# Performance work log

Hardware: AMD Instinct MI355X
Metric: run time of the kernel (lower is better)

## Reference

```python
import jax, jax.numpy as jnp
from jax import lax
import numpy as np

B, N, K = 8, 4096, 64          # clouds, points per cloud, max neighbors
N1, N2 = N // 2, N // 8        # fps ratio 0.5, then 0.25
R1, R2 = 0.2, 0.4              # ball-query radii


def setup_inputs() -> dict:
    key = jax.random.key(0)
    ks = jax.random.split(key, 7)
    def w(k, i, o):
        return jax.random.normal(k, (i, o), jnp.float32) / np.sqrt(i).astype(np.float32)
    return {
        "pos": jax.random.uniform(ks[0], (B, N, 3), jnp.float32),
        "w1a": w(ks[1], 3, 64),    "b1a": jnp.zeros(64, jnp.float32),
        "w1b": w(ks[2], 64, 64),   "b1b": jnp.zeros(64, jnp.float32),
        "w2a": w(ks[3], 67, 128),  "b2a": jnp.zeros(128, jnp.float32),
        "w2b": w(ks[4], 128, 128), "b2b": jnp.zeros(128, jnp.float32),
        "w3a": w(ks[5], 131, 256), "b3a": jnp.zeros(256, jnp.float32),
        "w3b": w(ks[6], 256, 1024),"b3b": jnp.zeros(1024, jnp.float32),
    }


def fps(pos, n_samples):
    # farthest point sampling, deterministic start at index 0. pos: [n, 3]
    d0 = jnp.sum((pos - pos[0]) ** 2, axis=-1)
    def step(mind, _):
        nxt = jnp.argmax(mind)
        d = jnp.sum((pos - pos[nxt]) ** 2, axis=-1)
        return jnp.minimum(mind, d), nxt
    _, idxs = lax.scan(step, d0, None, length=n_samples - 1)
    return jnp.concatenate([jnp.zeros((1,), idxs.dtype), idxs])


def ball_query(centers, pts, r):
    # up to K neighbors within radius r (nearest-first); centers are a subset of pts
    d2 = jnp.sum((centers[:, None, :] - pts[None, :, :]) ** 2, axis=-1)  # [M, n]
    neg = jnp.where(d2 <= r * r, -d2, -jnp.inf)
    vals, nbr = lax.top_k(neg, K)
    return nbr, vals > -jnp.inf  # [M, K] indices, validity mask


def mlp(x, w1, b1, w2, b2, relu_last):
    h = jax.nn.relu(x @ w1 + b1) @ w2 + b2
    return jax.nn.relu(h) if relu_last else h


def masked_max(h, mask):
    # max over neighbor axis; every center has itself as a valid neighbor
    return jnp.max(jnp.where(mask[..., None], h, -jnp.inf), axis=1)


def reference(pos, w1a, b1a, w1b, b1b, w2a, b2a, w2b, b2b, w3a, b3a, w3b, b3b):
    def single(p):  # p: [N, 3]
        # SA1: x is None -> per-edge input is relative position only
        idx1 = fps(p, N1)
        c1 = p[idx1]                                   # [N1, 3]
        nbr1, m1 = ball_query(c1, p, R1)               # [N1, K]
        rel1 = p[nbr1] - c1[:, None, :]                # [N1, K, 3]
        x1 = masked_max(mlp(rel1, w1a, b1a, w1b, b1b, True), m1)   # [N1, 64]
        # SA2: per-edge input is [x_j, pos_j - pos_i]
        idx2 = fps(c1, N2)
        c2 = c1[idx2]                                  # [N2, 3]
        nbr2, m2 = ball_query(c2, c1, R2)              # [N2, K]
        feat2 = jnp.concatenate([x1[nbr2], c1[nbr2] - c2[:, None, :]], axis=-1)  # [N2,K,67]
        x2 = masked_max(mlp(feat2, w2a, b2a, w2b, b2b, True), m2)  # [N2, 128]
        # Global SA: MLP on [x, pos] then global max pool
        g = mlp(jnp.concatenate([x2, c2], axis=-1), w3a, b3a, w3b, b3b, False)   # [N2,1024]
        return jnp.max(g, axis=0)                      # [1024]
    return jax.vmap(single)(pos)                       # [B, 1024]
```

## Files before the change

### kernel.cpp

```cpp
#include <hip/hip_runtime.h>
#include <cstdint>
#include <cstddef>


static constexpr int Bc = 8;
static constexpr int Np = 4096;
static constexpr int Kn = 64;
static constexpr int M1 = 2048;
static constexpr int M2 = 512;
static constexpr int LDX = 132;

#define DEVINL __device__ __forceinline__

DEVINL float d2_exact(float ax, float ay, float az, float bx, float by, float bz) {
    float dx = __fsub_rn(ax, bx);
    float dy = __fsub_rn(ay, by);
    float dz = __fsub_rn(az, bz);
    float xx = __fmul_rn(dx, dx);
    float yy = __fmul_rn(dy, dy);
    float zz = __fmul_rn(dz, dz);
    return __fadd_rn(__fadd_rn(xx, yy), zz);
}

template <int CTRL, int RM, int BM>
DEVINL unsigned long long dpp_max_step(unsigned long long k) {
    unsigned lo = (unsigned)k, hi = (unsigned)(k >> 32);
    unsigned slo = (unsigned)__builtin_amdgcn_update_dpp(0, (int)lo, CTRL, RM, BM, true);
    unsigned shi = (unsigned)__builtin_amdgcn_update_dpp(0, (int)hi, CTRL, RM, BM, true);
    unsigned long long s = ((unsigned long long)shi << 32) | (unsigned long long)slo;
    return s > k ? s : k;
}

DEVINL unsigned long long wave_max_u64_dpp(unsigned long long k) {
    k = dpp_max_step<0x111, 0xf, 0xf>(k);
    k = dpp_max_step<0x112, 0xf, 0xf>(k);
    k = dpp_max_step<0x114, 0xf, 0xf>(k);
    k = dpp_max_step<0x118, 0xf, 0xf>(k);
    k = dpp_max_step<0x142, 0xa, 0xf>(k);
    k = dpp_max_step<0x143, 0xc, 0xf>(k);
    return k;
}

DEVINL unsigned mort3(unsigned v) {
    return (v & 1u) | ((v & 2u) << 2) | ((v & 4u) << 4);
}

DEVINL unsigned cell_of(float x, float y, float z) {
    int ix = (int)(x * 8.0f); ix = ix < 0 ? 0 : (ix > 7 ? 7 : ix);
    int iy = (int)(y * 8.0f); iy = iy < 0 ? 0 : (iy > 7 ? 7 : iy);
    int iz = (int)(z * 8.0f); iz = iz < 0 ? 0 : (iz > 7 ? 7 : iz);
    return mort3((unsigned)ix) | (mort3((unsigned)iy) << 1) | (mort3((unsigned)iz) << 2);
}

DEVINL unsigned* scan512(unsigned* h0, unsigned* h1, int t) {
    unsigned* src = h0; unsigned* dst = h1;
    for (int d = 1; d < 512; d <<= 1) {
        unsigned v = src[t];
        if (t >= d) v += src[t - d];
        dst[t] = v;
        __syncthreads();
        unsigned* tmp = src; src = dst; dst = tmp;
    }
    return src;
}

__global__ __launch_bounds__(512)
void fps2x_kernel(const float* __restrict__ pos, float* __restrict__ c1,
                  float* __restrict__ c2, float* __restrict__ X) {
    constexpr int NT = 512;
    __shared__ float scx[Np], scy[Np], scz[Np];
    __shared__ unsigned spk[Np];
    __shared__ float s2c[M1 * 3];
    __shared__ unsigned h0[512], h1[512];
    __shared__ unsigned long long slots[3];
    const int b = blockIdx.x;
    const int t = threadIdx.x;
    const int lane = t & 63;

    {
        constexpr int PT = Np / NT;
        const float* base = pos + (size_t)b * Np * 3;
        float gx[PT], gy[PT], gz[PT];
        unsigned gc[PT];
        #pragma unroll
        for (int j = 0; j < PT; ++j) {
            int p = j * NT + t;
            gx[j] = base[p * 3 + 0];
            gy[j] = base[p * 3 + 1];
            gz[j] = base[p * 3 + 2];
            gc[j] = cell_of(gx[j], gy[j], gz[j]);
        }
        float x0 = base[0], y0 = base[1], z0 = base[2];
        h0[t] = 0;
        if (t == 0) { slots[0] = 0; slots[1] = 0; slots[2] = 0; }
        __syncthreads();
        #pragma unroll
        for (int j = 0; j < PT; ++j) atomicAdd(&h0[gc[j]], 1u);
        __syncthreads();
        unsigned cnt = h0[t];
        unsigned* inc = scan512(h0, h1, t);
        inc[t] -= cnt;
        __syncthreads();
        #pragma unroll
        for (int j = 0; j < PT; ++j) {
            unsigned p = atomicAdd(&inc[gc[j]], 1u);
            scx[p] = gx[j]; scy[p] = gy[j]; scz[p] = gz[j];
            spk[p] = ((0xFFFu - (unsigned)(j * NT + t)) << 12) | p;
        }
        __syncthreads();

        float px[PT], py[PT], pz[PT], mind[PT];
        unsigned oi[PT];
        #pragma unroll
        for (int j = 0; j < PT; ++j) {
            int p = t * PT + j;
            px[j] = scx[p]; py[j] = scy[p]; pz[j] = scz[p];
            oi[j] = spk[p];
        }
        float lox = px[0], hix = px[0], loy = py[0], hiy = py[0], loz = pz[0], hiz = pz[0];
        #pragma unroll
        for (int j = 1; j < PT; ++j) {
            lox = fminf(lox, px[j]); hix = fmaxf(hix, px[j]);
            loy = fminf(loy, py[j]); hiy = fmaxf(hiy, py[j]);
            loz = fminf(loz, pz[j]); hiz = fmaxf(hiz, pz[j]);
        }

        unsigned long long ck = 0;
        #pragma unroll
        for (int j = 0; j < PT; ++j) {
            float d = d2_exact(px[j], py[j], pz[j], x0, y0, z0);
            mind[j] = d;
            unsigned long long kj =
                ((unsigned long long)__float_as_uint(d) << 24) | (unsigned long long)oi[j];
            if (kj > ck) ck = kj;
        }
        float bmax = __uint_as_float((unsigned)(ck >> 24));
        unsigned long long wkey = wave_max_u64_dpp(ck);
        if (lane == 63) atomicMax(&slots[1], wkey);
        if (t == 0) {
            c1[((size_t)b * M1) * 3 + 0] = x0;
            c1[((size_t)b * M1) * 3 + 1] = y0;
            c1[((size_t)b * M1) * 3 + 2] = z0;
            s2c[0] = x0; s2c[1] = y0; s2c[2] = z0;
        }
        int rd = 1, wr = 2, rs = 0;
        for (int s = 1; s < M1; ++s) {
            __syncthreads();
            unsigned long long km = slots[rd];
            if (t == 0) slots[rs] = 0;
            unsigned spos = (unsigned)km & 0xFFFu;
            float cx = scx[spos], cy = scy[spos], cz = scz[spos];
            if (t == 0) {
                c1[((size_t)b * M1 + s) * 3 + 0] = cx;
                c1[((size_t)b * M1 + s) * 3 + 1] = cy;
                c1[((size_t)b * M1 + s) * 3 + 2] = cz;
                s2c[s * 3 + 0] = cx; s2c[s * 3 + 1] = cy; s2c[s * 3 + 2] = cz;
            }
            float dxv = fmaxf(fmaxf(lox - cx, cx - hix), 0.0f);
            float dyv = fmaxf(fmaxf(loy - cy, cy - hiy), 0.0f);
            float dzv = fmaxf(fmaxf(loz - cz, cz - hiz), 0.0f);
            float L = dxv * dxv + dyv * dyv + dzv * dzv;
            bool fire = (L * 0.999f <= bmax);
            if (fire) {
                unsigned long long nck = 0;
                #pragma unroll
                for (int j = 0; j < PT; ++j) {
                    float d = d2_exact(px[j], py[j], pz[j], cx, cy, cz);
                    float m = fminf(mind[j], d);
                    mind[j] = m;
                    unsigned long long kj =
                        ((unsigned long long)__float_as_uint(m) << 24) | (unsigned long long)oi[j];
                    if (kj > nck) nck = kj;
                }
                ck = nck;
                bmax = __uint_as_float((unsigned)(ck >> 24));
            }
            if (__ballot(fire) != 0ull) wkey = wave_max_u64_dpp(ck);
            if (lane == 63) atomicMax(&slots[wr], wkey);
            int nrd = wr; wr = rs; rs = rd; rd = nrd;
        }
    }
    __syncthreads();

    {
        constexpr int PT = M1 / NT;
        float gx[PT], gy[PT], gz[PT];
        unsigned gc[PT];
        #pragma unroll
        for (int j = 0; j < PT; ++j) {
            int p = j * NT + t;
            gx[j] = s2c[p * 3 + 0];
            gy[j] = s2c[p * 3 + 1];
            gz[j] = s2c[p * 3 + 2];
            gc[j] = cell_of(gx[j], gy[j], gz[j]);
        }
        float x0 = s2c[0], y0 = s2c[1], z0 = s2c[2];
        h0[t] = 0;
        if (t == 0) { slots[0] = 0; slots[1] = 0; slots[2] = 0; }
        __syncthreads();
        #pragma unroll
        for (int j = 0; j < PT; ++j) atomicAdd(&h0[gc[j]], 1u);
        __syncthreads();
        unsigned cnt = h0[t];
        unsigned* inc = scan512(h0, h1, t);
        inc[t] -= cnt;
        __syncthreads();
        #pragma unroll
        for (int j = 0; j < PT; ++j) {
            unsigned p = atomicAdd(&inc[gc[j]], 1u);
            scx[p] = gx[j]; scy[p] = gy[j]; scz[p] = gz[j];
            spk[p] = ((0xFFFu - (unsigned)(j * NT + t)) << 12) | p;
        }
        __syncthreads();

        float px[PT], py[PT], pz[PT], mind[PT];
        unsigned oi[PT];
        #pragma unroll
        for (int j = 0; j < PT; ++j) {
            int p = t * PT + j;
            px[j] = scx[p]; py[j] = scy[p]; pz[j] = scz[p];
            oi[j] = spk[p];
        }
        float lox = px[0], hix = px[0], loy = py[0], hiy = py[0], loz = pz[0], hiz = pz[0];
        #pragma unroll
        for (int j = 1; j < PT; ++j) {
            lox = fminf(lox, px[j]); hix = fmaxf(hix, px[j]);
            loy = fminf(loy, py[j]); hiy = fmaxf(hiy, py[j]);
            loz = fminf(loz, pz[j]); hiz = fmaxf(hiz, pz[j]);
        }

        unsigned long long ck = 0;
        #pragma unroll
        for (int j = 0; j < PT; ++j) {
            float d = d2_exact(px[j], py[j], pz[j], x0, y0, z0);
            mind[j] = d;
            unsigned long long kj =
                ((unsigned long long)__float_as_uint(d) << 24) | (unsigned long long)oi[j];
            if (kj > ck) ck = kj;
        }
        float bmax = __uint_as_float((unsigned)(ck >> 24));
        unsigned long long wkey = wave_max_u64_dpp(ck);
        if (lane == 63) atomicMax(&slots[1], wkey);
        if (t == 0) {
            c2[((size_t)b * M2) * 3 + 0] = x0;
            c2[((size_t)b * M2) * 3 + 1] = y0;
            c2[((size_t)b * M2) * 3 + 2] = z0;
            float* xr = X + (size_t)(b * M2) * LDX;
            xr[128] = x0; xr[129] = y0; xr[130] = z0;
        }
        int rd = 1, wr = 2, rs = 0;
        for (int s = 1; s < M2; ++s) {
            __syncthreads();
            unsigned long long km = slots[rd];
            if (t == 0) slots[rs] = 0;
            unsigned spos = (unsigned)km & 0xFFFu;
            float cx = scx[spos], cy = scy[spos], cz = scz[spos];
            if (t == 0) {
                c2[((size_t)b * M2 + s) * 3 + 0] = cx;
                c2[((size_t)b * M2 + s) * 3 + 1] = cy;
                c2[((size_t)b * M2 + s) * 3 + 2] = cz;
                float* xr = X + (size_t)(b * M2 + s) * LDX;
                xr[128] = cx; xr[129] = cy; xr[130] = cz;
            }
            float dxv = fmaxf(fmaxf(lox - cx, cx - hix), 0.0f);
            float dyv = fmaxf(fmaxf(loy - cy, cy - hiy), 0.0f);
            float dzv = fmaxf(fmaxf(loz - cz, cz - hiz), 0.0f);
            float L = dxv * dxv + dyv * dyv + dzv * dzv;
            bool fire = (L * 0.999f <= bmax);
            if (fire) {
                unsigned long long nck = 0;
                #pragma unroll
                for (int j = 0; j < PT; ++j) {
                    float d = d2_exact(px[j], py[j], pz[j], cx, cy, cz);
                    float m = fminf(mind[j], d);
                    mind[j] = m;
                    unsigned long long kj =
                        ((unsigned long long)__float_as_uint(m) << 24) | (unsigned long long)oi[j];
                    if (kj > nck) nck = kj;
                }
                ck = nck;
                bmax = __uint_as_float((unsigned)(ck >> 24));
            }
            if (__ballot(fire) != 0ull) wkey = wave_max_u64_dpp(ck);
            if (lane == 63) atomicMax(&slots[wr], wkey);
            int nrd = wr; wr = rs; rs = rd; rd = nrd;
        }
    }
}

template <int NPT>
__global__ __launch_bounds__(256)
void bq_kernel(const float* __restrict__ pts, const float* __restrict__ ctr,
               int mshift, float r2, int* __restrict__ nbr) {
    constexpr int CH = NPT / 64;
    constexpr int CAP = 1024;
    __shared__ uint2 cbuf[4][CAP];
    const int lane = threadIdx.x & 63;
    const int wl = threadIdx.x >> 6;
    int w = __builtin_amdgcn_readfirstlane((int)(blockIdx.x * 4 + wl));
    const int b = w >> mshift;
    const float* pb = pts + (size_t)b * NPT * 3;
    const float* cp = ctr + (size_t)w * 3;
    float cx = cp[0], cy = cp[1], cz = cp[2];
    const unsigned r2b = __float_as_uint(r2);

    unsigned ub[CH];
    int cnt = 0;
    #pragma unroll
    for (int j = 0; j < CH; ++j) {
        int p = j * 64 + lane;
        float d = d2_exact(pb[p * 3 + 0], pb[p * 3 + 1], pb[p * 3 + 2], cx, cy, cz);
        ub[j] = __float_as_uint(d);
        cnt += __popcll(__ballot(ub[j] <= r2b));
    }
    int* out = nbr + (size_t)w * Kn;
    const unsigned long long lml = (1ull << lane) - 1ull;

    if (cnt <= Kn) {
        int basep = 0;
        #pragma unroll
        for (int j = 0; j < CH; ++j) {
            bool v = ub[j] <= r2b;
            unsigned long long mk = __ballot(v);
            if (v) out[basep + __popcll(mk & lml)] = j * 64 + lane;
            basep += __popcll(mk);
        }
        if (lane >= cnt) out[lane] = -1;
    } else if (cnt <= CAP) {
        uint2* buf = cbuf[wl];
        int basep = 0;
        #pragma unroll
        for (int j = 0; j < CH; ++j) {
            bool v = ub[j] <= r2b;
            unsigned long long mk = __ballot(v);
            if (v) buf[basep + __popcll(mk & lml)] =
                       make_uint2(ub[j], (unsigned)(j * 64 + lane));
            basep += __popcll(mk);
        }
        const int C2 = (cnt + 63) >> 6;
        unsigned cb[CAP / 64], ci[CAP / 64];
        #pragma unroll
        for (int e = 0; e < CAP / 64; ++e) {
            if (e >= C2) break;
            int p = e * 64 + lane;
            uint2 v = buf[p];
            cb[e] = (p < cnt) ? v.x : 0xFFFFFFFFu;
            ci[e] = v.y;
        }
        unsigned lo = 0, hi = r2b;
        while (lo < hi) {
            unsigned mid = lo + ((hi - lo) >> 1);
            int c = 0;
            #pragma unroll
            for (int e = 0; e < CAP / 64; ++e) {
                if (e >= C2) break;
                c += __popcll(__ballot(cb[e] <= mid));
            }
            if (c >= Kn) hi = mid; else lo = mid + 1;
        }
        const unsigned tt = lo;
        int cntLess = 0;
        #pragma unroll
        for (int e = 0; e < CAP / 64; ++e) {
            if (e >= C2) break;
            cntLess += __popcll(__ballot(cb[e] < tt));
        }
        const int quota = Kn - cntLess;
        int baseLt = 0, eqseen = 0;
        #pragma unroll
        for (int e = 0; e < CAP / 64; ++e) {
            if (e >= C2) break;
            bool lt = cb[e] < tt;
            bool eq = cb[e] == tt;
            unsigned long long mlt = __ballot(lt);
            unsigned long long meq = __ballot(eq);
            if (lt) out[baseLt + __popcll(mlt & lml)] = (int)ci[e];
            if (eq) {
                int rr = eqseen + __popcll(meq & lml);
                if (rr < quota) out[cntLess + rr] = (int)ci[e];
            }
            baseLt += __popcll(mlt);
            eqseen += __popcll(meq);
        }
    } else {
        unsigned lo = 0, hi = r2b;
        while (lo < hi) {
            unsigned mid = lo + ((hi - lo) >> 1);
            int c = 0;
            #pragma unroll
            for (int j = 0; j < CH; ++j) c += __popcll(__ballot(ub[j] <= mid));
            if (c >= Kn) hi = mid; else lo = mid + 1;
        }
        const unsigned tt = lo;
        int cntLess = 0;
        #pragma unroll
        for (int j = 0; j < CH; ++j) cntLess += __popcll(__ballot(ub[j] < tt));
        const int quota = Kn - cntLess;
        int baseLt = 0, eqseen = 0;
        #pragma unroll
        for (int j = 0; j < CH; ++j) {
            bool lt = ub[j] < tt;
            bool eq = ub[j] == tt;
            unsigned long long mlt = __ballot(lt);
            unsigned long long meq = __ballot(eq);
            if (lt) out[baseLt + __popcll(mlt & lml)] = j * 64 + lane;
            if (eq) {
                int rr = eqseen + __popcll(meq & lml);
                if (rr < quota) out[cntLess + rr] = j * 64 + lane;
            }
            baseLt += __popcll(mlt);
            eqseen += __popcll(meq);
        }
    }
}

__global__ __launch_bounds__(256)
void mlp1_kernel(const float* __restrict__ pos, const float* __restrict__ c1,
                 const int* __restrict__ nbr, const float* __restrict__ w1aT,
                 const float* __restrict__ w1bT, const float* __restrict__ b1b,
                 float* __restrict__ x1) {
    const int lane = threadIdx.x & 63;
    int w = __builtin_amdgcn_readfirstlane((int)(blockIdx.x * 4 + (threadIdx.x >> 6)));
    const int b = w >> 11;
    const int ii = nbr[(size_t)w * Kn + lane];
    const bool valid = ii >= 0;
    const int i2 = valid ? ii : 0;
    const float* pp = pos + ((size_t)b * Np + i2) * 3;
    const float* cc = c1 + (size_t)w * 3;
    float rx = pp[0] - cc[0], ry = pp[1] - cc[1], rz = pp[2] - cc[2];
    float h1[64];
    #pragma unroll
    for (int h = 0; h < 64; ++h) {
        float4 wv = ((const float4*)w1aT)[h];
        float a = fmaf(rx, wv.x, fmaf(ry, wv.y, fmaf(rz, wv.z, wv.w)));
        h1[h] = fmaxf(a, 0.0f);
    }
    float* orow = x1 + (size_t)w * 64;
    for (int c4 = 0; c4 < 16; ++c4) {
        float v4[4];
        #pragma unroll
        for (int cq = 0; cq < 4; ++cq) {
            int c = c4 * 4 + cq;
            float acc = b1b[c];
            const float4* wr = (const float4*)(w1bT + (size_t)c * 64);
            #pragma unroll
            for (int q = 0; q < 16; ++q) {
                float4 wv = wr[q];
                acc = fmaf(h1[4 * q + 0], wv.x, acc);
                acc = fmaf(h1[4 * q + 1], wv.y, acc);
                acc = fmaf(h1[4 * q + 2], wv.z, acc);
                acc = fmaf(h1[4 * q + 3], wv.w, acc);
            }
            float v = fmaxf(acc, 0.0f);
            v = valid ? v : -__builtin_inff();
            #pragma unroll
            for (int o = 32; o > 0; o >>= 1) v = fmaxf(v, __shfl_xor(v, o, 64));
            v4[cq] = v;
        }
        if (lane == 0)
            ((float4*)orow)[c4] = make_float4(v4[0], v4[1], v4[2], v4[3]);
    }
}

__global__ __launch_bounds__(256)
void mlp2_kernel(const float* __restrict__ x1, const float* __restrict__ c1,
                 const float* __restrict__ c2, const int* __restrict__ nbr2,
                 const float* __restrict__ w2aT, const float* __restrict__ w2bT,
                 const float* __restrict__ b2b, float* __restrict__ X) {
    const int lane = threadIdx.x & 63;
    int w = __builtin_amdgcn_readfirstlane((int)(blockIdx.x * 4 + (threadIdx.x >> 6)));
    const int b = w >> 9;
    const int ii = nbr2[(size_t)w * Kn + lane];
    const bool valid = ii >= 0;
    const int i2 = valid ? ii : 0;

    float x[68];
    const float4* xr = (const float4*)(x1 + ((size_t)b * M1 + i2) * 64);
    #pragma unroll
    for (int q = 0; q < 16; ++q) {
        float4 v = xr[q];
        x[4 * q + 0] = v.x; x[4 * q + 1] = v.y;
        x[4 * q + 2] = v.z; x[4 * q + 3] = v.w;
    }
    const float* cc = c2 + (size_t)w * 3;
    const float* cp = c1 + ((size_t)b * M1 + i2) * 3;
    x[64] = cp[0] - cc[0];
    x[65] = cp[1] - cc[1];
    x[66] = cp[2] - cc[2];
    x[67] = 0.0f;

    float h1[128];
    #pragma unroll
    for (int h = 0; h < 128; ++h) {
        const float4* r4 = (const float4*)(w2aT + (size_t)h * 80);
        float acc = 0.0f;
        #pragma unroll
        for (int q = 0; q < 16; ++q) {
            float4 wv = r4[q];
            acc = fmaf(x[4 * q + 0], wv.x, acc);
            acc = fmaf(x[4 * q + 1], wv.y, acc);
            acc = fmaf(x[4 * q + 2], wv.z, acc);
            acc = fmaf(x[4 * q + 3], wv.w, acc);
        }
        float4 tl = r4[16];
        acc = fmaf(x[64], tl.x, acc);
        acc = fmaf(x[65], tl.y, acc);
        acc = fmaf(x[66], tl.z, acc);
        acc += tl.w;
        h1[h] = fmaxf(acc, 0.0f);
    }
    float* orow = X + (size_t)w * LDX;
    for (int c4 = 0; c4 < 32; ++c4) {
        float v4[4];
        #pragma unroll
        for (int cq = 0; cq < 4; ++cq) {
            int c = c4 * 4 + cq;
            float acc = b2b[c];
            const float4* wr = (const float4*)(w2bT + (size_t)c * 128);
            #pragma unroll
            for (int q = 0; q < 32; ++q) {
                float4 wv = wr[q];
                acc = fmaf(h1[4 * q + 0], wv.x, acc);
                acc = fmaf(h1[4 * q + 1], wv.y, acc);
                acc = fmaf(h1[4 * q + 2], wv.z, acc);
                acc = fmaf(h1[4 * q + 3], wv.w, acc);
            }
            float v = fmaxf(acc, 0.0f);
            v = valid ? v : -__builtin_inff();
            #pragma unroll
            for (int o = 32; o > 0; o >>= 1) v = fmaxf(v, __shfl_xor(v, o, 64));
            v4[cq] = v;
        }
        if (lane == 0) {
            orow[c4 * 4 + 0] = v4[0]; orow[c4 * 4 + 1] = v4[1];
            orow[c4 * 4 + 2] = v4[2]; orow[c4 * 4 + 3] = v4[3];
        }
    }
}

__global__ __launch_bounds__(256)
void gemm1_kernel(const float* __restrict__ X, const float* __restrict__ w3a,
                  const float* __restrict__ b3a, float* __restrict__ H) {
    const int r = blockIdx.x;
    const int c = threadIdx.x;
    const float* xr = X + (size_t)r * LDX;
    float acc = b3a[c];
    for (int i = 0; i < 131; ++i)
        acc = fmaf(xr[i], w3a[(size_t)i * 256 + c], acc);
    H[(size_t)r * 256 + c] = fmaxf(acc, 0.0f);
}

__global__ __launch_bounds__(256)
void gemm2_kernel(const float* __restrict__ H, const float* __restrict__ w3b,
                  float* __restrict__ part) {
    __shared__ float As[32][33];
    __shared__ float Bs[32][64];
    __shared__ float red[8][64];
    const int bidx = blockIdx.x;
    const int nt = bidx & 15;
    const int mt = (bidx >> 4) & 15;
    const int b = bidx >> 8;
    const int row0 = b * M2 + mt * 32;
    const int col0 = nt * 64;
    const int t = threadIdx.x;
    const int rg = t >> 5, cg = t & 31;

    float acc[4][2] = {{0.f, 0.f}, {0.f, 0.f}, {0.f, 0.f}, {0.f, 0.f}};
    for (int k0 = 0; k0 < 256; k0 += 32) {
        #pragma unroll
        for (int q = 0; q < 4; ++q) {
            int id = t + q * 256;
            As[id >> 5][id & 31] = H[(size_t)(row0 + (id >> 5)) * 256 + k0 + (id & 31)];
        }
        #pragma unroll
        for (int q = 0; q < 8; ++q) {
            int id = t + q * 256;
            Bs[id >> 6][id & 63] = w3b[(size_t)(k0 + (id >> 6)) * 1024 + col0 + (id & 63)];
        }
        __syncthreads();
        #pragma unroll
        for (int kk = 0; kk < 32; ++kk) {
            float b0 = Bs[kk][cg * 2 + 0];
            float b1 = Bs[kk][cg * 2 + 1];
            #pragma unroll
            for (int j = 0; j < 4; ++j) {
                float a = As[rg * 4 + j][kk];
                acc[j][0] = fmaf(a, b0, acc[j][0]);
                acc[j][1] = fmaf(a, b1, acc[j][1]);
            }
        }
        __syncthreads();
    }
    float m0 = fmaxf(fmaxf(acc[0][0], acc[1][0]), fmaxf(acc[2][0], acc[3][0]));
    float m1 = fmaxf(fmaxf(acc[0][1], acc[1][1]), fmaxf(acc[2][1], acc[3][1]));
    red[rg][cg * 2 + 0] = m0;
    red[rg][cg * 2 + 1] = m1;
    __syncthreads();
    if (t < 64) {
        float v = red[0][t];
        #pragma unroll
        for (int q = 1; q < 8; ++q) v = fmaxf(v, red[q][t]);
        part[((size_t)b * 16 + mt) * 1024 + col0 + t] = v;
    }
}

__global__ __launch_bounds__(256)
void rmax_kernel(const float* __restrict__ part, const float* __restrict__ b3b,
                 float* __restrict__ out) {
    int i = blockIdx.x * 256 + threadIdx.x;
    int b = i >> 10, c = i & 1023;
    float v = -__builtin_inff();
    #pragma unroll
    for (int tt = 0; tt < 16; ++tt)
        v = fmaxf(v, part[((size_t)b * 16 + tt) * 1024 + c]);
    out[i] = v + b3b[c];
}

__global__ __launch_bounds__(256)
void prep_kernel(const float* __restrict__ w1a, const float* __restrict__ b1a,
                 const float* __restrict__ w1b, const float* __restrict__ w2a,
                 const float* __restrict__ b2a, const float* __restrict__ w2b,
                 float* __restrict__ w1aT, float* __restrict__ w1bT,
                 float* __restrict__ w2aT, float* __restrict__ w2bT) {
    int i = blockIdx.x * 256 + threadIdx.x;
    if (i < 64 * 4) {
        int h = i >> 2, d = i & 3;
        w1aT[i] = (d < 3) ? w1a[d * 64 + h] : b1a[h];
    }
    if (i < 64 * 64) {
        int c = i >> 6, h = i & 63;
        w1bT[i] = w1b[h * 64 + c];
    }
    if (i < 128 * 80) {
        int h = i / 80, d = i - h * 80;
        w2aT[i] = (d < 67) ? w2a[d * 128 + h] : ((d == 67) ? b2a[h] : 0.0f);
    }
    {
        int c = i >> 7, h = i & 127;
        w2bT[i] = w2b[h * 128 + c];
    }
}

extern "C" void kernel_launch(void* const* d_in, const int* in_sizes, int n_in,
                              void* d_out, int out_size, void* d_ws, size_t ws_size,
                              hipStream_t stream) {
    const float* pos = (const float*)d_in[0];
    const float* w1a = (const float*)d_in[1];
    const float* b1a = (const float*)d_in[2];
    const float* w1b = (const float*)d_in[3];
    const float* b1b = (const float*)d_in[4];
    const float* w2a = (const float*)d_in[5];
    const float* b2a = (const float*)d_in[6];
    const float* w2b = (const float*)d_in[7];
    const float* b2b = (const float*)d_in[8];
    const float* w3a = (const float*)d_in[9];
    const float* b3a = (const float*)d_in[10];
    const float* w3b = (const float*)d_in[11];
    const float* b3b = (const float*)d_in[12];
    float* out = (float*)d_out;

    char* ws = (char*)d_ws;
    size_t off = 0;
    auto alloc = [&](size_t bytes) -> char* {
        char* p = ws + off;
        off += (bytes + 255) & ~(size_t)255;
        return p;
    };
    float* c1   = (float*)alloc(sizeof(float) * Bc * M1 * 3);
    float* c2   = (float*)alloc(sizeof(float) * Bc * M2 * 3);
    int*   nbr1 = (int*)alloc(sizeof(int) * Bc * M1 * Kn);
    int*   nbr2 = (int*)alloc(sizeof(int) * Bc * M2 * Kn);
    float* x1   = (float*)alloc(sizeof(float) * Bc * M1 * 64);
    float* X    = (float*)alloc(sizeof(float) * Bc * M2 * LDX);
    float* H    = (float*)alloc(sizeof(float) * Bc * M2 * 256);
    float* part = (float*)alloc(sizeof(float) * Bc * 16 * 1024);
    float* w1aT = (float*)alloc(sizeof(float) * 64 * 4);
    float* w1bT = (float*)alloc(sizeof(float) * 64 * 64);
    float* w2aT = (float*)alloc(sizeof(float) * 128 * 80);
    float* w2bT = (float*)alloc(sizeof(float) * 128 * 128);

    prep_kernel<<<dim3(64), dim3(256), 0, stream>>>(w1a, b1a, w1b, w2a, b2a, w2b,
                                                    w1aT, w1bT, w2aT, w2bT);
    fps2x_kernel<<<dim3(Bc), dim3(512), 0, stream>>>(pos, c1, c2, X);
    bq_kernel<Np><<<dim3(Bc * M1 / 4), dim3(256), 0, stream>>>(
        pos, c1, 11, (float)(0.2 * 0.2), nbr1);
    mlp1_kernel<<<dim3(Bc * M1 / 4), dim3(256), 0, stream>>>(
        pos, c1, nbr1, w1aT, w1bT, b1b, x1);
    bq_kernel<M1><<<dim3(Bc * M2 / 4), dim3(256), 0, stream>>>(
        c1, c2, 9, (float)(0.4 * 0.4), nbr2);
    mlp2_kernel<<<dim3(Bc * M2 / 4), dim3(256), 0, stream>>>(
        x1, c1, c2, nbr2, w2aT, w2bT, b2b, X);
    gemm1_kernel<<<dim3(Bc * M2), dim3(256), 0, stream>>>(X, w3a, b3a, H);
    gemm2_kernel<<<dim3(Bc * 16 * 16), dim3(256), 0, stream>>>(H, w3b, part);
    rmax_kernel<<<dim3(32), dim3(256), 0, stream>>>(part, b3b, out);
}
```

Measured before the change: 2.501 ms.

## Fuse FPS, ball query, MLPs into persistent mega-kernel with progress flags

Replaces the separate FPS, ball-query, MLP and first global GEMM kernels with one persistent kernel of 256 blocks. The first 8 blocks to take a ticket run farthest point sampling and publish progress counters every 64 centers with release stores. The other blocks pull work items from atomic queues and spin-wait on those counters, so ball query and MLP work for early centers overlaps the serial FPS. This removes launch gaps and the nbr and X intermediate buffers, but it depends on the FPS blocks being resident and risks deadlock or contention from spinning blocks and higher register pressure.

```diff
diff --git a/kernel.cpp b/kernel.cpp
--- a/kernel.cpp
+++ b/kernel.cpp
@@ -8,9 +8,15 @@
 static constexpr int Kn = 64;
 static constexpr int M1 = 2048;
 static constexpr int M2 = 512;
-static constexpr int LDX = 132;
 
 #define DEVINL __device__ __forceinline__
+
+#define CTRL_P1 0
+#define CTRL_P2 8
+#define CTRL_D1 16
+#define CTRL_TK 24
+#define CTRL_Q1 25
+#define CTRL_Q2 26
 
 DEVINL float d2_exact(float ax, float ay, float az, float bx, float by, float bz) {
     float dx = __fsub_rn(ax, bx);
@@ -64,490 +70,520 @@
     return src;
 }
 
-__global__ __launch_bounds__(512)
-void fps2x_kernel(const float* __restrict__ pos, float* __restrict__ c1,
-                  float* __restrict__ c2, float* __restrict__ X) {
+DEVINL unsigned acq_load(const unsigned* p) {
+    return __hip_atomic_load(p, __ATOMIC_ACQUIRE, __HIP_MEMORY_SCOPE_AGENT);
+}
+
+__global__ __launch_bounds__(512, 2)
+void mega_kernel(const float* __restrict__ pos, float* __restrict__ c1,
+                 float* __restrict__ c2, float* __restrict__ x1,
+                 float* __restrict__ H,
+                 const float* __restrict__ w1aT, const float* __restrict__ w1bT,
+                 const float* __restrict__ b1b, const float* __restrict__ w2aT,
+                 const float* __restrict__ w2bT, const float* __restrict__ b2b,
+                 const float* __restrict__ w3a, const float* __restrict__ b3a,
+                 unsigned* __restrict__ ctrl) {
     constexpr int NT = 512;
     __shared__ float scx[Np], scy[Np], scz[Np];
     __shared__ unsigned spk[Np];
     __shared__ float s2c[M1 * 3];
-    __shared__ unsigned h0[512], h1[512];
+    __shared__ unsigned h0[512], h1s[512];
     __shared__ unsigned long long slots[3];
-    const int b = blockIdx.x;
+    __shared__ int nout[8][Kn];
+    __shared__ float xrow[8][128];
+    __shared__ int roleSh;
     const int t = threadIdx.x;
     const int lane = t & 63;
-
-    {
-        constexpr int PT = Np / NT;
-        const float* base = pos + (size_t)b * Np * 3;
-        float gx[PT], gy[PT], gz[PT];
-        unsigned gc[PT];
-        #pragma unroll
-        for (int j = 0; j < PT; ++j) {
-            int p = j * NT + t;
-            gx[j] = base[p * 3 + 0];
-            gy[j] = base[p * 3 + 1];
-            gz[j] = base[p * 3 + 2];
-            gc[j] = cell_of(gx[j], gy[j], gz[j]);
-        }
-        float x0 = base[0], y0 = base[1], z0 = base[2];
-        h0[t] = 0;
-        if (t == 0) { slots[0] = 0; slots[1] = 0; slots[2] = 0; }
-        __syncthreads();
-        #pragma unroll
-        for (int j = 0; j < PT; ++j) atomicAdd(&h0[gc[j]], 1u);
-        __syncthreads();
-        unsigned cnt = h0[t];
-        unsigned* inc = scan512(h0, h1, t);
-        inc[t] -= cnt;
-        __syncthreads();
-        #pragma unroll
-        for (int j = 0; j < PT; ++j) {
-            unsigned p = atomicAdd(&inc[gc[j]], 1u);
-            scx[p] = gx[j]; scy[p] = gy[j]; scz[p] = gz[j];
-            spk[p] = ((0xFFFu - (unsigned)(j * NT + t)) << 12) | p;
+    const int wl = t >> 6;
+
+    if (t == 0) roleSh = (int)atomicAdd(&ctrl[CTRL_TK], 1u);
+    __syncthreads();
+    const int role = roleSh;
+
+    if (role < Bc) {
+        const int b = role;
+        {
+            constexpr int PT = Np / NT;
+            const float* base = pos + (size_t)b * Np * 3;
+            float gx[PT], gy[PT], gz[PT];
+            unsigned gc[PT];
+            #pragma unroll
+            for (int j = 0; j < PT; ++j) {
+                int p = j * NT + t;
+                gx[j] = base[p * 3 + 0];
+                gy[j] = base[p * 3 + 1];
+                gz[j] = base[p * 3 + 2];
+                gc[j] = cell_of(gx[j], gy[j], gz[j]);
+            }
+            float x0 = base[0], y0 = base[1], z0 = base[2];
+            h0[t] = 0;
+            if (t == 0) { slots[0] = 0; slots[1] = 0; slots[2] = 0; }
+            __syncthreads();
+            #pragma unroll
+            for (int j = 0; j < PT; ++j) atomicAdd(&h0[gc[j]], 1u);
+            __syncthreads();
+            unsigned cnt = h0[t];
+            unsigned* inc = scan512(h0, h1s, t);
+            inc[t] -= cnt;
+            __syncthreads();
+            #pragma unroll
+            for (int j = 0; j < PT; ++j) {
+                unsigned p = atomicAdd(&inc[gc[j]], 1u);
+                scx[p] = gx[j]; scy[p] = gy[j]; scz[p] = gz[j];
+                spk[p] = ((0xFFFu - (unsigned)(j * NT + t)) << 12) | p;
+            }
+            __syncthreads();
+
+            float px[PT], py[PT], pz[PT], mind[PT];
+            unsigned oi[PT];
+            #pragma unroll
+            for (int j = 0; j < PT; ++j) {
+                int p = t * PT + j;
+                px[j] = scx[p]; py[j] = scy[p]; pz[j] = scz[p];
+                oi[j] = spk[p];
+            }
+            float lox = px[0], hix = px[0], loy = py[0], hiy = py[0], loz = pz[0], hiz = pz[0];
+            #pragma unroll
+            for (int j = 1; j < PT; ++j) {
+                lox = fminf(lox, px[j]); hix = fmaxf(hix, px[j]);
+                loy = fminf(loy, py[j]); hiy = fmaxf(hiy, py[j]);
+                loz = fminf(loz, pz[j]); hiz = fmaxf(hiz, pz[j]);
+            }
+
+            unsigned long long ck = 0;
+            #pragma unroll
+            for (int j = 0; j < PT; ++j) {
+                float d = d2_exact(px[j], py[j], pz[j], x0, y0, z0);
+                mind[j] = d;
+                unsigned long long kj =
+                    ((unsigned long long)__float_as_uint(d) << 24) | (unsigned long long)oi[j];
+                if (kj > ck) ck = kj;
+            }
+            float bmax = __uint_as_float((unsigned)(ck >> 24));
+            unsigned long long wkey = wave_max_u64_dpp(ck);
+            if (lane == 63) atomicMax(&slots[1], wkey);
+            if (t == 0) {
+                c1[((size_t)b * M1) * 3 + 0] = x0;
+                c1[((size_t)b * M1) * 3 + 1] = y0;
+                c1[((size_t)b * M1) * 3 + 2] = z0;
+                s2c[0] = x0; s2c[1] = y0; s2c[2] = z0;
+            }
+            int rd = 1, wr = 2, rs = 0;
+            for (int s = 1; s < M1; ++s) {
+                __syncthreads();
+                unsigned long long km = slots[rd];
+                if (t == 0) slots[rs] = 0;
+                unsigned spos = (unsigned)km & 0xFFFu;
+                float cx = scx[spos], cy = scy[spos], cz = scz[spos];
+                if (t == 0) {
+                    c1[((size_t)b * M1 + s) * 3 + 0] = cx;
+                    c1[((size_t)b * M1 + s) * 3 + 1] = cy;
+                    c1[((size_t)b * M1 + s) * 3 + 2] = cz;
+                    s2c[s * 3 + 0] = cx; s2c[s * 3 + 1] = cy; s2c[s * 3 + 2] = cz;
+                    if ((s & 63) == 63)
+                        __hip_atomic_store(&ctrl[CTRL_P1 + b], (unsigned)(s + 1),
+                                           __ATOMIC_RELEASE, __HIP_MEMORY_SCOPE_AGENT);
+                }
+                float dxv = fmaxf(fmaxf(lox - cx, cx - hix), 0.0f);
+                float dyv = fmaxf(fmaxf(loy - cy, cy - hiy), 0.0f);
+                float dzv = fmaxf(fmaxf(loz - cz, cz - hiz), 0.0f);
+                float L = dxv * dxv + dyv * dyv + dzv * dzv;
+                bool fire = (L * 0.999f <= bmax);
+                if (fire) {
+                    unsigned long long nck = 0;
+                    #pragma unroll
+                    for (int j = 0; j < PT; ++j) {
+                        float d = d2_exact(px[j], py[j], pz[j], cx, cy, cz);
+                        float m = fminf(mind[j], d);
+                        mind[j] = m;
+                        unsigned long long kj =
+                            ((unsigned long long)__float_as_uint(m) << 24) | (unsigned long long)oi[j];
+                        if (kj > nck) nck = kj;
+                    }
+                    ck = nck;
+                    bmax = __uint_as_float((unsigned)(ck >> 24));
+                }
+                if (__ballot(fire) != 0ull) wkey = wave_max_u64_dpp(ck);
+                if (lane == 63) atomicMax(&slots[wr], wkey);
+                int nrd = wr; wr = rs; rs = rd; rd = nrd;
+            }
         }
         __syncthreads();
 
-        float px[PT], py[PT], pz[PT], mind[PT];
-        unsigned oi[PT];
-        #pragma unroll
-        for (int j = 0; j < PT; ++j) {
-            int p = t * PT + j;
-            px[j] = scx[p]; py[j] = scy[p]; pz[j] = scz[p];
-            oi[j] = spk[p];
+        {
+            constexpr int PT = M1 / NT;
+            float gx[PT], gy[PT], gz[PT];
+            unsigned gc[PT];
+            #pragma unroll
+            for (int j = 0; j < PT; ++j) {
+                int p = j * NT + t;
+                gx[j] = s2c[p * 3 + 0];
+                gy[j] = s2c[p * 3 + 1];
+                gz[j] = s2c[p * 3 + 2];
+                gc[j] = cell_of(gx[j], gy[j], gz[j]);
+            }
+            float x0 = s2c[0], y0 = s2c[1], z0 = s2c[2];
+            h0[t] = 0;
+            if (t == 0) { slots[0] = 0; slots[1] = 0; slots[2] = 0; }
+            __syncthreads();
+            #pragma unroll
+            for (int j = 0; j < PT; ++j) atomicAdd(&h0[gc[j]], 1u);
+            __syncthreads();
+            unsigned cnt = h0[t];
+            unsigned* inc = scan512(h0, h1s, t);
+            inc[t] -= cnt;
+            __syncthreads();
+            #pragma unroll
+            for (int j = 0; j < PT; ++j) {
+                unsigned p = atomicAdd(&inc[gc[j]], 1u);
+                scx[p] = gx[j]; scy[p] = gy[j]; scz[p] = gz[j];
+                spk[p] = ((0xFFFu - (unsigned)(j * NT + t)) << 12) | p;
+            }
+            __syncthreads();
+
+            float px[PT], py[PT], pz[PT], mind[PT];
+            unsigned oi[PT];
+            #pragma unroll
+            for (int j = 0; j < PT; ++j) {
+                int p = t * PT + j;
+                px[j] = scx[p]; py[j] = scy[p]; pz[j] = scz[p];
+                oi[j] = spk[p];
+            }
+            float lox = px[0], hix = px[0], loy = py[0], hiy = py[0], loz = pz[0], hiz = pz[0];
+            #pragma unroll
+            for (int j = 1; j < PT; ++j) {
+                lox = fminf(lox, px[j]); hix = fmaxf(hix, px[j]);
+                loy = fminf(loy, py[j]); hiy = fmaxf(hiy, py[j]);
+                loz = fminf(loz, pz[j]); hiz = fmaxf(hiz, pz[j]);
+            }
+
+            unsigned long long ck = 0;
+            #pragma unroll
+            for (int j = 0; j < PT; ++j) {
+                float d = d2_exact(px[j], py[j], pz[j], x0, y0, z0);
+                mind[j] = d;
+                unsigned long long kj =
+                    ((unsigned long long)__float_as_uint(d) << 24) | (unsigned long long)oi[j];
+                if (kj > ck) ck = kj;
+            }
+            float bmax = __uint_as_float((unsigned)(ck >> 24));
+            unsigned long long wkey = wave_max_u64_dpp(ck);
+            if (lane == 63) atomicMax(&slots[1], wkey);
+            if (t == 0) {
+                c2[((size_t)b * M2) * 3 + 0] = x0;
+                c2[((size_t)b * M2) * 3 + 1] = y0;
+                c2[((size_t)b * M2) * 3 + 2] = z0;
+            }
+            int rd = 1, wr = 2, rs = 0;
+            for (int s = 1; s < M2; ++s) {
+                __syncthreads();
+                unsigned long long km = slots[rd];
+                if (t == 0) slots[rs] = 0;
+                unsigned spos = (unsigned)km & 0xFFFu;
+                float cx = scx[spos], cy = scy[spos], cz = scz[spos];
+                if (t == 0) {
+                    c2[((size_t)b * M2 + s) * 3 + 0] = cx;
+                    c2[((size_t)b * M2 + s) * 3 + 1] = cy;
+                    c2[((size_t)b * M2 + s) * 3 + 2] = cz;
+                    if ((s & 63) == 63)
+                        __hip_atomic_store(&ctrl[CTRL_P2 + b], (unsigned)(s + 1),
+                                           __ATOMIC_RELEASE, __HIP_MEMORY_SCOPE_AGENT);
+                }
+                float dxv = fmaxf(fmaxf(lox - cx, cx - hix), 0.0f);
+                float dyv = fmaxf(fmaxf(loy - cy, cy - hiy), 0.0f);
+                float dzv = fmaxf(fmaxf(loz - cz, cz - hiz), 0.0f);
+                float L = dxv * dxv + dyv * dyv + dzv * dzv;
+                bool fire = (L * 0.999f <= bmax);
+                if (fire) {
+                    unsigned long long nck = 0;
+                    #pragma unroll
+                    for (int j = 0; j < PT; ++j) {
+                        float d = d2_exact(px[j], py[j], pz[j], cx, cy, cz);
+                        float m = fminf(mind[j], d);
+                        mind[j] = m;
+                        unsigned long long kj =
+                            ((unsigned long long)__float_as_uint(m) << 24) | (unsigned long long)oi[j];
+                        if (kj > nck) nck = kj;
+                    }
+                    ck = nck;
+                    bmax = __uint_as_float((unsigned)(ck >> 24));
+                }
+                if (__ballot(fire) != 0ull) wkey = wave_max_u64_dpp(ck);
+                if (lane == 63) atomicMax(&slots[wr], wkey);
+                int nrd = wr; wr = rs; rs = rd; rd = nrd;
+            }
         }
-        float lox = px[0], hix = px[0], loy = py[0], hiy = py[0], loz = pz[0], hiz = pz[0];
-        #pragma unroll
-        for (int j = 1; j < PT; ++j) {
-            lox = fminf(lox, px[j]); hix = fmaxf(hix, px[j]);
-            loy = fminf(loy, py[j]); hiy = fmaxf(hiy, py[j]);
-            loz = fminf(loz, pz[j]); hiz = fmaxf(hiz, pz[j]);
+    }
+
+    const unsigned long long lml = (1ull << lane) - 1ull;
+    {
+        const unsigned r2b = __float_as_uint((float)(0.2 * 0.2));
+        for (;;) {
+            int widx;
+            if (lane == 0) widx = (int)atomicAdd(&ctrl[CTRL_Q1], 1u);
+            widx = __shfl(widx, 0, 64);
+            if (widx >= Bc * M1) break;
+            const int cb = widx & 7;
+            const int cs = widx >> 3;
+            while (acq_load(&ctrl[CTRL_P1 + cb]) <= (unsigned)cs)
+                __builtin_amdgcn_s_sleep(32);
+            const int w = cb * M1 + cs;
+            const float* cp = c1 + (size_t)w * 3;
+            float cx = cp[0], cy = cp[1], cz = cp[2];
+            const float* pb = pos + (size_t)cb * Np * 3;
+            unsigned ub[64];
+            int cnt = 0;
+            #pragma unroll
+            for (int j = 0; j < 64; ++j) {
+                int p = j * 64 + lane;
+                float d = d2_exact(pb[p * 3 + 0], pb[p * 3 + 1], pb[p * 3 + 2], cx, cy, cz);
+                ub[j] = __float_as_uint(d);
+                cnt += __popcll(__ballot(ub[j] <= r2b));
+            }
+            int* out = &nout[wl][0];
+            if (cnt <= Kn) {
+                int basep = 0;
+                #pragma unroll
+                for (int j = 0; j < 64; ++j) {
+                    bool v = ub[j] <= r2b;
+                    unsigned long long mk = __ballot(v);
+                    if (v) out[basep + __popcll(mk & lml)] = j * 64 + lane;
+                    basep += __popcll(mk);
+                }
+                if (lane >= cnt) out[lane] = -1;
+            } else {
+                unsigned lo = 0, hi = r2b;
+                while (lo < hi) {
+                    unsigned mid = lo + ((hi - lo) >> 1);
+                    int c = 0;
+                    #pragma unroll
+                    for (int j = 0; j < 64; ++j) c += __popcll(__ballot(ub[j] <= mid));
+                    if (c >= Kn) hi = mid; else lo = mid + 1;
+                }
+                const unsigned tt = lo;
+                int cntLess = 0;
+                #pragma unroll
+                for (int j = 0; j < 64; ++j) cntLess += __popcll(__ballot(ub[j] < tt));
+                const int quota = Kn - cntLess;
+                int baseLt = 0, eqseen = 0;
+                #pragma unroll
+                for (int j = 0; j < 64; ++j) {
+                    bool lt = ub[j] < tt;
+                    bool eq = ub[j] == tt;
+                    unsigned long long mlt = __ballot(lt);
+                    unsigned long long meq = __ballot(eq);
+                    if (lt) out[baseLt + __popcll(mlt & lml)] = j * 64 + lane;
+                    if (eq) {
+                        int rr = eqseen + __popcll(meq & lml);
+                        if (rr < quota) out[cntLess + rr] = j * 64 + lane;
+                    }
+                    baseLt += __popcll(mlt);
+                    eqseen += __popcll(meq);
+                }
+            }
+            const int ii = out[lane];
+            const bool valid = ii >= 0;
+            const int i2 = valid ? ii : 0;
+            const float* pp = pos + ((size_t)cb * Np + i2) * 3;
+            float rx = pp[0] - cx, ry = pp[1] - cy, rz = pp[2] - cz;
+            float h1[64];
+            #pragma unroll
+            for (int h = 0; h < 64; ++h) {
+                float4 wv = ((const float4*)w1aT)[h];
+                float a = fmaf(rx, wv.x, fmaf(ry, wv.y, fmaf(rz, wv.z, wv.w)));
+                h1[h] = fmaxf(a, 0.0f);
+            }
+            float* orow = x1 + (size_t)w * 64;
+            for (int c4 = 0; c4 < 16; ++c4) {
+                float v4[4];
+                #pragma unroll
+                for (int cq = 0; cq < 4; ++cq) {
+                    int c = c4 * 4 + cq;
+                    float acc = b1b[c];
+                    const float4* wr = (const float4*)(w1bT + (size_t)c * 64);
+                    #pragma unroll
+                    for (int q = 0; q < 16; ++q) {
+                        float4 wv = wr[q];
+                        acc = fmaf(h1[4 * q + 0], wv.x, acc);
+                        acc = fmaf(h1[4 * q + 1], wv.y, acc);
+                        acc = fmaf(h1[4 * q + 2], wv.z, acc);
+                        acc = fmaf(h1[4 * q + 3], wv.w, acc);
+                    }
+                    float v = fmaxf(acc, 0.0f);
+                    v = valid ? v : -__builtin_inff();
+                    #pragma unroll
+                    for (int o = 32; o > 0; o >>= 1) v = fmaxf(v, __shfl_xor(v, o, 64));
+                    v4[cq] = v;
+                }
+                if (lane == 0)
+                    ((float4*)orow)[c4] = make_float4(v4[0], v4[1], v4[2], v4[3]);
+            }
+            if (lane == 0)
+                __hip_atomic_fetch_add(&ctrl[CTRL_D1 + cb], 1u,
+                                       __ATOMIC_RELEASE, __HIP_MEMORY_SCOPE_AGENT);
         }
-
-        unsigned long long ck = 0;
-        #pragma unroll
-        for (int j = 0; j < PT; ++j) {
-            float d = d2_exact(px[j], py[j], pz[j], x0, y0, z0);
-            mind[j] = d;
-            unsigned long long kj =
-                ((unsigned long long)__float_as_uint(d) << 24) | (unsigned long long)oi[j];
-            if (kj > ck) ck = kj;
+    }
+
+    {
+        const unsigned r2b = __float_as_uint((float)(0.4 * 0.4));
+        for (;;) {
+            int widx;
+            if (lane == 0) widx = (int)atomicAdd(&ctrl[CTRL_Q2], 1u);
+            widx = __shfl(widx, 0, 64);
+            if (widx >= Bc * M2) break;
+            const int cb = widx & 7;
+            const int cs = widx >> 3;
+            while (acq_load(&ctrl[CTRL_P2 + cb]) <= (unsigned)cs)
+                __builtin_amdgcn_s_sleep(32);
+            while (acq_load(&ctrl[CTRL_D1 + cb]) < (unsigned)M1)
+                __builtin_amdgcn_s_sleep(32);
+            const int w = cb * M2 + cs;
+            const float* ccp = c2 + (size_t)w * 3;
+            float cx = ccp[0], cy = ccp[1], cz = ccp[2];
+            const float* pb = c1 + (size_t)cb * M1 * 3;
+            unsigned ub[32];
+            int cnt = 0;
+            #pragma unroll
+            for (int j = 0; j < 32; ++j) {
+                int p = j * 64 + lane;
+                float d = d2_exact(pb[p * 3 + 0], pb[p * 3 + 1], pb[p * 3 + 2], cx, cy, cz);
+                ub[j] = __float_as_uint(d);
+                cnt += __popcll(__ballot(ub[j] <= r2b));
+            }
+            int* out = &nout[wl][0];
+            if (cnt <= Kn) {
+                int basep = 0;
+                #pragma unroll
+                for (int j = 0; j < 32; ++j) {
+                    bool v = ub[j] <= r2b;
+                    unsigned long long mk = __ballot(v);
+                    if (v) out[basep + __popcll(mk & lml)] = j * 64 + lane;
+                    basep += __popcll(mk);
+                }
+                if (lane >= cnt) out[lane] = -1;
+            } else {
+                unsigned lo = 0, hi = r2b;
+                while (lo < hi) {
+                    unsigned mid = lo + ((hi - lo) >> 1);
+                    int c = 0;
+                    #pragma unroll
+                    for (int j = 0; j < 32; ++j) c += __popcll(__ballot(ub[j] <= mid));
+                    if (c >= Kn) hi = mid; else lo = mid + 1;
+                }
+                const unsigned tt = lo;
+                int cntLess = 0;
+                #pragma unroll
+                for (int j = 0; j < 32; ++j) cntLess += __popcll(__ballot(ub[j] < tt));
+                const int quota = Kn - cntLess;
+                int baseLt = 0, eqseen = 0;
+                #pragma unroll
+                for (int j = 0; j < 32; ++j) {
+                    bool lt = ub[j] < tt;
+                    bool eq = ub[j] == tt;
+                    unsigned long long mlt = __ballot(lt);
+                    unsigned long long meq = __ballot(eq);
+                    if (lt) out[baseLt + __popcll(mlt & lml)] = j * 64 + lane;
+                    if (eq) {
+                        int rr = eqseen + __popcll(meq & lml);
+                        if (rr < quota) out[cntLess + rr] = j * 64 + lane;
+                    }
+                    baseLt += __popcll(mlt);
+                    eqseen += __popcll(meq);
+                }
+            }
+            {
+                const int ii = out[lane];
+                const bool valid = ii >= 0;
+                const int i2 = valid ? ii : 0;
+                float x[68];
+                const float4* xr = (const float4*)(x1 + ((size_t)cb * M1 + i2) * 64);
+                #pragma unroll
+                for (int q = 0; q < 16; ++q) {
+                    float4 v = xr[q];
+                    x[4 * q + 0] = v.x; x[4 * q + 1] = v.y;
+                    x[4 * q + 2] = v.z; x[4 * q + 3] = v.w;
+                }
+                const float* cpn = c1 + ((size_t)cb * M1 + i2) * 3;
+                x[64] = cpn[0] - cx;
+                x[65] = cpn[1] - cy;
+                x[66] = cpn[2] - cz;
+                x[67] = 0.0f;
+                float h1[128];
+                #pragma unroll
+                for (int h = 0; h < 128; ++h) {
+                    const float4* r4 = (const float4*)(w2aT + (size_t)h * 80);
+                    float acc = 0.0f;
+                    #pragma unroll
+                    for (int q = 0; q < 16; ++q) {
+                        float4 wv = r4[q];
+                        acc = fmaf(x[4 * q + 0], wv.x, acc);
+                        acc = fmaf(x[4 * q + 1], wv.y, acc);
+                        acc = fmaf(x[4 * q + 2], wv.z, acc);
+                        acc = fmaf(x[4 * q + 3], wv.w, acc);
+                    }
+                    float4 tl = r4[16];
+                    acc = fmaf(x[64], tl.x, acc);
+                    acc = fmaf(x[65], tl.y, acc);
+                    acc = fmaf(x[66], tl.z, acc);
+                    acc += tl.w;
+                    h1[h] = fmaxf(acc, 0.0f);
+                }
+                for (int c4 = 0; c4 < 32; ++c4) {
+                    float v4[4];
+                    #pragma unroll
+                    for (int cq = 0; cq < 4; ++cq) {
+                        int c = c4 * 4 + cq;
+                        float acc = b2b[c];
+                        const float4* wr = (const float4*)(w2bT + (size_t)c * 128);
+                        #pragma unroll
+                        for (int q = 0; q < 32; ++q) {
+                            float4 wv = wr[q];
+                            acc = fmaf(h1[4 * q + 0], wv.x, acc);
+                            acc = fmaf(h1[4 * q + 1], wv.y, acc);
+                            acc = fmaf(h1[4 * q + 2], wv.z, acc);
+                            acc = fmaf(h1[4 * q + 3], wv.w, acc);
+                        }
+                        float v = fmaxf(acc, 0.0f);
+                        v = valid ? v : -__builtin_inff();
+                        #pragma unroll
+                        for (int o = 32; o > 0; o >>= 1) v = fmaxf(v, __shfl_xor(v, o, 64));
+                        v4[cq] = v;
+                    }
+                    if (lane == 0) {
+                        xrow[wl][c4 * 4 + 0] = v4[0]; xrow[wl][c4 * 4 + 1] = v4[1];
+                        xrow[wl][c4 * 4 + 2] = v4[2]; xrow[wl][c4 * 4 + 3] = v4[3];
+                    }
+                }
+            }
+            {
+                const int c0 = lane * 4;
+                float4 bias = *(const float4*)(b3a + c0);
+                float a0 = bias.x, a1 = bias.y, a2 = bias.z, a3 = bias.w;
+                for (int i = 0; i < 128; ++i) {
+                    float xv = xrow[wl][i];
+                    float4 wv = *(const float4*)(w3a + (size_t)i * 256 + c0);
+                    a0 = fmaf(xv, wv.x, a0);
+                    a1 = fmaf(xv, wv.y, a1);
+                    a2 = fmaf(xv, wv.z, a2);
+                    a3 = fmaf(xv, wv.w, a3);
+                }
+                {
+                    float4 wv = *(const float4*)(w3a + (size_t)128 * 256 + c0);
+                    a0 = fmaf(cx, wv.x, a0); a1 = fmaf(cx, wv.y, a1);
+                    a2 = fmaf(cx, wv.z, a2); a3 = fmaf(cx, wv.w, a3);
+                    wv = *(const float4*)(w3a + (size_t)129 * 256 + c0);
+                    a0 = fmaf(cy, wv.x, a0); a1 = fmaf(cy, wv.y, a1);
+                    a2 = fmaf(cy, wv.z, a2); a3 = fmaf(cy, wv.w, a3);
+                    wv = *(const float4*)(w3a + (size_t)130 * 256 + c0);
+                    a0 = fmaf(cz, wv.x, a0); a1 = fmaf(cz, wv.y, a1);
+                    a2 = fmaf(cz, wv.z, a2); a3 = fmaf(cz, wv.w, a3);
+                }
+                *(float4*)(H + (size_t)w * 256 + c0) =
+                    make_float4(fmaxf(a0, 0.0f), fmaxf(a1, 0.0f),
+                                fmaxf(a2, 0.0f), fmaxf(a3, 0.0f));
+            }
         }
-        float bmax = __uint_as_float((unsigned)(ck >> 24));
-        unsigned long long wkey = wave_max_u64_dpp(ck);
-        if (lane == 63) atomicMax(&slots[1], wkey);
-        if (t == 0) {
-            c1[((size_t)b * M1) * 3 + 0] = x0;
-            c1[((size_t)b * M1) * 3 + 1] = y0;
-            c1[((size_t)b * M1) * 3 + 2] = z0;
-            s2c[0] = x0; s2c[1] = y0; s2c[2] = z0;
-        }
-        int rd = 1, wr = 2, rs = 0;
-        for (int s = 1; s < M1; ++s) {
-            __syncthreads();
-            unsigned long long km = slots[rd];
-            if (t == 0) slots[rs] = 0;
-            unsigned spos = (unsigned)km & 0xFFFu;
-            float cx = scx[spos], cy = scy[spos], cz = scz[spos];
-            if (t == 0) {
-                c1[((size_t)b * M1 + s) * 3 + 0] = cx;
-                c1[((size_t)b * M1 + s) * 3 + 1] = cy;
-                c1[((size_t)b * M1 + s) * 3 + 2] = cz;
-                s2c[s * 3 + 0] = cx; s2c[s * 3 + 1] = cy; s2c[s * 3 + 2] = cz;
-            }
-            float dxv = fmaxf(fmaxf(lox - cx, cx - hix), 0.0f);
-            float dyv = fmaxf(fmaxf(loy - cy, cy - hiy), 0.0f);
-            float dzv = fmaxf(fmaxf(loz - cz, cz - hiz), 0.0f);
-            float L = dxv * dxv + dyv * dyv + dzv * dzv;
-            bool fire = (L * 0.999f <= bmax);
-            if (fire) {
-                unsigned long long nck = 0;
-                #pragma unroll
-                for (int j = 0; j < PT; ++j) {
-                    float d = d2_exact(px[j], py[j], pz[j], cx, cy, cz);
-                    float m = fminf(mind[j], d);
-                    mind[j] = m;
-                    unsigned long long kj =
-                        ((unsigned long long)__float_as_uint(m) << 24) | (unsigned long long)oi[j];
-                    if (kj > nck) nck = kj;
-                }
-                ck = nck;
-                bmax = __uint_as_float((unsigned)(ck >> 24));
-            }
-            if (__ballot(fire) != 0ull) wkey = wave_max_u64_dpp(ck);
-            if (lane == 63) atomicMax(&slots[wr], wkey);
-            int nrd = wr; wr = rs; rs = rd; rd = nrd;
-        }
-    }
-    __syncthreads();
-
-    {
-        constexpr int PT = M1 / NT;
-        float gx[PT], gy[PT], gz[PT];
-        unsigned gc[PT];
-        #pragma unroll
-        for (int j = 0; j < PT; ++j) {
-            int p = j * NT + t;
-            gx[j] = s2c[p * 3 + 0];
-            gy[j] = s2c[p * 3 + 1];
-            gz[j] = s2c[p * 3 + 2];
-            gc[j] = cell_of(gx[j], gy[j], gz[j]);
-        }
-        float x0 = s2c[0], y0 = s2c[1], z0 = s2c[2];
-        h0[t] = 0;
-        if (t == 0) { slots[0] = 0; slots[1] = 0; slots[2] = 0; }
-        __syncthreads();
-        #pragma unroll
-        for (int j = 0; j < PT; ++j) atomicAdd(&h0[gc[j]], 1u);
-        __syncthreads();
-        unsigned cnt = h0[t];
-        unsigned* inc = scan512(h0, h1, t);
-        inc[t] -= cnt;
-        __syncthreads();
-        #pragma unroll
-        for (int j = 0; j < PT; ++j) {
-            unsigned p = atomicAdd(&inc[gc[j]], 1u);
-            scx[p] = gx[j]; scy[p] = gy[j]; scz[p] = gz[j];
-            spk[p] = ((0xFFFu - (unsigned)(j * NT + t)) << 12) | p;
-        }
-        __syncthreads();
-
-        float px[PT], py[PT], pz[PT], mind[PT];
-        unsigned oi[PT];
-        #pragma unroll
-        for (int j = 0; j < PT; ++j) {
-            int p = t * PT + j;
-            px[j] = scx[p]; py[j] = scy[p]; pz[j] = scz[p];
-            oi[j] = spk[p];
-        }
-        float lox = px[0], hix = px[0], loy = py[0], hiy = py[0], loz = pz[0], hiz = pz[0];
-        #pragma unroll
-        for (int j = 1; j < PT; ++j) {
-            lox = fminf(lox, px[j]); hix = fmaxf(hix, px[j]);
-            loy = fminf(loy, py[j]); hiy = fmaxf(hiy, py[j]);
-            loz = fminf(loz, pz[j]); hiz = fmaxf(hiz, pz[j]);
-        }
-
-        unsigned long long ck = 0;
-        #pragma unroll
-        for (int j = 0; j < PT; ++j) {
-            float d = d2_exact(px[j], py[j], pz[j], x0, y0, z0);
-            mind[j] = d;
-            unsigned long long kj =
-                ((unsigned long long)__float_as_uint(d) << 24) | (unsigned long long)oi[j];
-            if (kj > ck) ck = kj;
-        }
-        float bmax = __uint_as_float((unsigned)(ck >> 24));
-        unsigned long long wkey = wave_max_u64_dpp(ck);
-        if (lane == 63) atomicMax(&slots[1], wkey);
-        if (t == 0) {
-            c2[((size_t)b * M2) * 3 + 0] = x0;
-            c2[((size_t)b * M2) * 3 + 1] = y0;
-            c2[((size_t)b * M2) * 3 + 2] = z0;
-            float* xr = X + (size_t)(b * M2) * LDX;
-            xr[128] = x0; xr[129] = y0; xr[130] = z0;
-        }
-        int rd = 1, wr = 2, rs = 0;
-        for (int s = 1; s < M2; ++s) {
-            __syncthreads();
-            unsigned long long km = slots[rd];
-            if (t == 0) slots[rs] = 0;
-            unsigned spos = (unsigned)km & 0xFFFu;
-            float cx = scx[spos], cy = scy[spos], cz = scz[spos];
-            if (t == 0) {
-                c2[((size_t)b * M2 + s) * 3 + 0] = cx;
-                c2[((size_t)b * M2 + s) * 3 + 1] = cy;
-                c2[((size_t)b * M2 + s) * 3 + 2] = cz;
-                float* xr = X + (size_t)(b * M2 + s) * LDX;
-                xr[128] = cx; xr[129] = cy; xr[130] = cz;
-            }
-            float dxv = fmaxf(fmaxf(lox - cx, cx - hix), 0.0f);
-            float dyv = fmaxf(fmaxf(loy - cy, cy - hiy), 0.0f);
-            float dzv = fmaxf(fmaxf(loz - cz, cz - hiz), 0.0f);
-            float L = dxv * dxv + dyv * dyv + dzv * dzv;
-            bool fire = (L * 0.999f <= bmax);
-            if (fire) {
-                unsigned long long nck = 0;
-                #pragma unroll
-                for (int j = 0; j < PT; ++j) {
-                    float d = d2_exact(px[j], py[j], pz[j], cx, cy, cz);
-                    float m = fminf(mind[j], d);
-                    mind[j] = m;
-                    unsigned long long kj =
-                        ((unsigned long long)__float_as_uint(m) << 24) | (unsigned long long)oi[j];
-                    if (kj > nck) nck = kj;
-                }
-                ck = nck;
-                bmax = __uint_as_float((unsigned)(ck >> 24));
-            }
-            if (__ballot(fire) != 0ull) wkey = wave_max_u64_dpp(ck);
-            if (lane == 63) atomicMax(&slots[wr], wkey);
-            int nrd = wr; wr = rs; rs = rd; rd = nrd;
-        }
-    }
-}
-
-template <int NPT>
-__global__ __launch_bounds__(256)
-void bq_kernel(const float* __restrict__ pts, const float* __restrict__ ctr,
-               int mshift, float r2, int* __restrict__ nbr) {
-    constexpr int CH = NPT / 64;
-    constexpr int CAP = 1024;
-    __shared__ uint2 cbuf[4][CAP];
-    const int lane = threadIdx.x & 63;
-    const int wl = threadIdx.x >> 6;
-    int w = __builtin_amdgcn_readfirstlane((int)(blockIdx.x * 4 + wl));
-    const int b = w >> mshift;
-    const float* pb = pts + (size_t)b * NPT * 3;
-    const float* cp = ctr + (size_t)w * 3;
-    float cx = cp[0], cy = cp[1], cz = cp[2];
-    const unsigned r2b = __float_as_uint(r2);
-
-    unsigned ub[CH];
-    int cnt = 0;
-    #pragma unroll
-    for (int j = 0; j < CH; ++j) {
-        int p = j * 64 + lane;
-        float d = d2_exact(pb[p * 3 + 0], pb[p * 3 + 1], pb[p * 3 + 2], cx, cy, cz);
-        ub[j] = __float_as_uint(d);
-        cnt += __popcll(__ballot(ub[j] <= r2b));
-    }
-    int* out = nbr + (size_t)w * Kn;
-    const unsigned long long lml = (1ull << lane) - 1ull;
-
-    if (cnt <= Kn) {
-        int basep = 0;
-        #pragma unroll
-        for (int j = 0; j < CH; ++j) {
-            bool v = ub[j] <= r2b;
-            unsigned long long mk = __ballot(v);
-            if (v) out[basep + __popcll(mk & lml)] = j * 64 + lane;
-            basep += __popcll(mk);
-        }
-        if (lane >= cnt) out[lane] = -1;
-    } else if (cnt <= CAP) {
-        uint2* buf = cbuf[wl];
-        int basep = 0;
-        #pragma unroll
-        for (int j = 0; j < CH; ++j) {
-            bool v = ub[j] <= r2b;
-            unsigned long long mk = __ballot(v);
-            if (v) buf[basep + __popcll(mk & lml)] =
-                       make_uint2(ub[j], (unsigned)(j * 64 + lane));
-            basep += __popcll(mk);
-        }
-        const int C2 = (cnt + 63) >> 6;
-        unsigned cb[CAP / 64], ci[CAP / 64];
-        #pragma unroll
-        for (int e = 0; e < CAP / 64; ++e) {
-            if (e >= C2) break;
-            int p = e * 64 + lane;
-            uint2 v = buf[p];
-            cb[e] = (p < cnt) ? v.x : 0xFFFFFFFFu;
-            ci[e] = v.y;
-        }
-        unsigned lo = 0, hi = r2b;
-        while (lo < hi) {
-            unsigned mid = lo + ((hi - lo) >> 1);
-            int c = 0;
-            #pragma unroll
-            for (int e = 0; e < CAP / 64; ++e) {
-                if (e >= C2) break;
-                c += __popcll(__ballot(cb[e] <= mid));
-            }
-            if (c >= Kn) hi = mid; else lo = mid + 1;
-        }
-        const unsigned tt = lo;
-        int cntLess = 0;
-        #pragma unroll
-        for (int e = 0; e < CAP / 64; ++e) {
-            if (e >= C2) break;
-            cntLess += __popcll(__ballot(cb[e] < tt));
-        }
-        const int quota = Kn - cntLess;
-        int baseLt = 0, eqseen = 0;
-        #pragma unroll
-        for (int e = 0; e < CAP / 64; ++e) {
-            if (e >= C2) break;
-            bool lt = cb[e] < tt;
-            bool eq = cb[e] == tt;
-            unsigned long long mlt = __ballot(lt);
-            unsigned long long meq = __ballot(eq);
-            if (lt) out[baseLt + __popcll(mlt & lml)] = (int)ci[e];
-            if (eq) {
-                int rr = eqseen + __popcll(meq & lml);
-                if (rr < quota) out[cntLess + rr] = (int)ci[e];
-            }
-            baseLt += __popcll(mlt);
-            eqseen += __popcll(meq);
-        }
-    } else {
-        unsigned lo = 0, hi = r2b;
-        while (lo < hi) {
-            unsigned mid = lo + ((hi - lo) >> 1);
-            int c = 0;
-            #pragma unroll
-            for (int j = 0; j < CH; ++j) c += __popcll(__ballot(ub[j] <= mid));
-            if (c >= Kn) hi = mid; else lo = mid + 1;
-        }
-        const unsigned tt = lo;
-        int cntLess = 0;
-        #pragma unroll
-        for (int j = 0; j < CH; ++j) cntLess += __popcll(__ballot(ub[j] < tt));
-        const int quota = Kn - cntLess;
-        int baseLt = 0, eqseen = 0;
-        #pragma unroll
-        for (int j = 0; j < CH; ++j) {
-            bool lt = ub[j] < tt;
-            bool eq = ub[j] == tt;
-            unsigned long long mlt = __ballot(lt);
-            unsigned long long meq = __ballot(eq);
-            if (lt) out[baseLt + __popcll(mlt & lml)] = j * 64 + lane;
-            if (eq) {
-                int rr = eqseen + __popcll(meq & lml);
-                if (rr < quota) out[cntLess + rr] = j * 64 + lane;
-            }
-            baseLt += __popcll(mlt);
-            eqseen += __popcll(meq);
-        }
-    }
-}
-
-__global__ __launch_bounds__(256)
-void mlp1_kernel(const float* __restrict__ pos, const float* __restrict__ c1,
-                 const int* __restrict__ nbr, const float* __restrict__ w1aT,
-                 const float* __restrict__ w1bT, const float* __restrict__ b1b,
-                 float* __restrict__ x1) {
-    const int lane = threadIdx.x & 63;
-    int w = __builtin_amdgcn_readfirstlane((int)(blockIdx.x * 4 + (threadIdx.x >> 6)));
-    const int b = w >> 11;
-    const int ii = nbr[(size_t)w * Kn + lane];
-    const bool valid = ii >= 0;
-    const int i2 = valid ? ii : 0;
-    const float* pp = pos + ((size_t)b * Np + i2) * 3;
-    const float* cc = c1 + (size_t)w * 3;
-    float rx = pp[0] - cc[0], ry = pp[1] - cc[1], rz = pp[2] - cc[2];
-    float h1[64];
-    #pragma unroll
-    for (int h = 0; h < 64; ++h) {
-        float4 wv = ((const float4*)w1aT)[h];
-        float a = fmaf(rx, wv.x, fmaf(ry, wv.y, fmaf(rz, wv.z, wv.w)));
-        h1[h] = fmaxf(a, 0.0f);
-    }
-    float* orow = x1 + (size_t)w * 64;
-    for (int c4 = 0; c4 < 16; ++c4) {
-        float v4[4];
-        #pragma unroll
-        for (int cq = 0; cq < 4; ++cq) {
-            int c = c4 * 4 + cq;
-            float acc = b1b[c];
-            const float4* wr = (const float4*)(w1bT + (size_t)c * 64);
-            #pragma unroll
-            for (int q = 0; q < 16; ++q) {
-                float4 wv = wr[q];
-                acc = fmaf(h1[4 * q + 0], wv.x, acc);
-                acc = fmaf(h1[4 * q + 1], wv.y, acc);
-                acc = fmaf(h1[4 * q + 2], wv.z, acc);
-                acc = fmaf(h1[4 * q + 3], wv.w, acc);
-            }
-            float v = fmaxf(acc, 0.0f);
-            v = valid ? v : -__builtin_inff();
-            #pragma unroll
-            for (int o = 32; o > 0; o >>= 1) v = fmaxf(v, __shfl_xor(v, o, 64));
-            v4[cq] = v;
-        }
-        if (lane == 0)
-            ((float4*)orow)[c4] = make_float4(v4[0], v4[1], v4[2], v4[3]);
-    }
-}
-
-__global__ __launch_bounds__(256)
-void mlp2_kernel(const float* __restrict__ x1, const float* __restrict__ c1,
-                 const float* __restrict__ c2, const int* __restrict__ nbr2,
-                 const float* __restrict__ w2aT, const float* __restrict__ w2bT,
-                 const float* __restrict__ b2b, float* __restrict__ X) {
-    const int lane = threadIdx.x & 63;
-    int w = __builtin_amdgcn_readfirstlane((int)(blockIdx.x * 4 + (threadIdx.x >> 6)));
-    const int b = w >> 9;
-    const int ii = nbr2[(size_t)w * Kn + lane];
-    const bool valid = ii >= 0;
-    const int i2 = valid ? ii : 0;
-
-    float x[68];
-    const float4* xr = (const float4*)(x1 + ((size_t)b * M1 + i2) * 64);
-    #pragma unroll
-    for (int q = 0; q < 16; ++q) {
-        float4 v = xr[q];
-        x[4 * q + 0] = v.x; x[4 * q + 1] = v.y;
-        x[4 * q + 2] = v.z; x[4 * q + 3] = v.w;
-    }
-    const float* cc = c2 + (size_t)w * 3;
-    const float* cp = c1 + ((size_t)b * M1 + i2) * 3;
-    x[64] = cp[0] - cc[0];
-    x[65] = cp[1] - cc[1];
-    x[66] = cp[2] - cc[2];
-    x[67] = 0.0f;
-
-    float h1[128];
-    #pragma unroll
-    for (int h = 0; h < 128; ++h) {
-        const float4* r4 = (const float4*)(w2aT + (size_t)h * 80);
-        float acc = 0.0f;
-        #pragma unroll
-        for (int q = 0; q < 16; ++q) {
-            float4 wv = r4[q];
-            acc = fmaf(x[4 * q + 0], wv.x, acc);
-            acc = fmaf(x[4 * q + 1], wv.y, acc);
-            acc = fmaf(x[4 * q + 2], wv.z, acc);
-            acc = fmaf(x[4 * q + 3], wv.w, acc);
-        }
-        float4 tl = r4[16];
-        acc = fmaf(x[64], tl.x, acc);
-        acc = fmaf(x[65], tl.y, acc);
-        acc = fmaf(x[66], tl.z, acc);
-        acc += tl.w;
-        h1[h] = fmaxf(acc, 0.0f);
-    }
-    float* orow = X + (size_t)w * LDX;
-    for (int c4 = 0; c4 < 32; ++c4) {
-        float v4[4];
-        #pragma unroll
-        for (int cq = 0; cq < 4; ++cq) {
-            int c = c4 * 4 + cq;
-            float acc = b2b[c];
-            const float4* wr = (const float4*)(w2bT + (size_t)c * 128);
-            #pragma unroll
-            for (int q = 0; q < 32; ++q) {
-                float4 wv = wr[q];
-                acc = fmaf(h1[4 * q + 0], wv.x, acc);
-                acc = fmaf(h1[4 * q + 1], wv.y, acc);
-                acc = fmaf(h1[4 * q + 2], wv.z, acc);
-                acc = fmaf(h1[4 * q + 3], wv.w, acc);
-            }
-            float v = fmaxf(acc, 0.0f);
-            v = valid ? v : -__builtin_inff();
-            #pragma unroll
-            for (int o = 32; o > 0; o >>= 1) v = fmaxf(v, __shfl_xor(v, o, 64));
-            v4[cq] = v;
-        }
-        if (lane == 0) {
-            orow[c4 * 4 + 0] = v4[0]; orow[c4 * 4 + 1] = v4[1];
-            orow[c4 * 4 + 2] = v4[2]; orow[c4 * 4 + 3] = v4[3];
-        }
-    }
-}
-
-__global__ __launch_bounds__(256)
-void gemm1_kernel(const float* __restrict__ X, const float* __restrict__ w3a,
-                  const float* __restrict__ b3a, float* __restrict__ H) {
-    const int r = blockIdx.x;
-    const int c = threadIdx.x;
-    const float* xr = X + (size_t)r * LDX;
-    float acc = b3a[c];
-    for (int i = 0; i < 131; ++i)
-        acc = fmaf(xr[i], w3a[(size_t)i * 256 + c], acc);
-    H[(size_t)r * 256 + c] = fmaxf(acc, 0.0f);
+    }
 }
 
 __global__ __launch_bounds__(256)
@@ -668,29 +704,20 @@
     };
     float* c1   = (float*)alloc(sizeof(float) * Bc * M1 * 3);
     float* c2   = (float*)alloc(sizeof(float) * Bc * M2 * 3);
-    int*   nbr1 = (int*)alloc(sizeof(int) * Bc * M1 * Kn);
-    int*   nbr2 = (int*)alloc(sizeof(int) * Bc * M2 * Kn);
     float* x1   = (float*)alloc(sizeof(float) * Bc * M1 * 64);
-    float* X    = (float*)alloc(sizeof(float) * Bc * M2 * LDX);
     float* H    = (float*)alloc(sizeof(float) * Bc * M2 * 256);
     float* part = (float*)alloc(sizeof(float) * Bc * 16 * 1024);
     float* w1aT = (float*)alloc(sizeof(float) * 64 * 4);
     float* w1bT = (float*)alloc(sizeof(float) * 64 * 64);
     float* w2aT = (float*)alloc(sizeof(float) * 128 * 80);
     float* w2bT = (float*)alloc(sizeof(float) * 128 * 128);
-
+    unsigned* ctrl = (unsigned*)alloc(256);
+
+    hipMemsetAsync(ctrl, 0, 256, stream);
     prep_kernel<<<dim3(64), dim3(256), 0, stream>>>(w1a, b1a, w1b, w2a, b2a, w2b,
                                                     w1aT, w1bT, w2aT, w2bT);
-    fps2x_kernel<<<dim3(Bc), dim3(512), 0, stream>>>(pos, c1, c2, X);
-    bq_kernel<Np><<<dim3(Bc * M1 / 4), dim3(256), 0, stream>>>(
-        pos, c1, 11, (float)(0.2 * 0.2), nbr1);
-    mlp1_kernel<<<dim3(Bc * M1 / 4), dim3(256), 0, stream>>>(
-        pos, c1, nbr1, w1aT, w1bT, b1b, x1);
-    bq_kernel<M1><<<dim3(Bc * M2 / 4), dim3(256), 0, stream>>>(
-        c1, c2, 9, (float)(0.4 * 0.4), nbr2);
-    mlp2_kernel<<<dim3(Bc * M2 / 4), dim3(256), 0, stream>>>(
-        x1, c1, c2, nbr2, w2aT, w2bT, b2b, X);
-    gemm1_kernel<<<dim3(Bc * M2), dim3(256), 0, stream>>>(X, w3a, b3a, H);
+    mega_kernel<<<dim3(256), dim3(512), 0, stream>>>(
+        pos, c1, c2, x1, H, w1aT, w1bT, b1b, w2aT, w2bT, b2b, w3a, b3a, ctrl);
     gemm2_kernel<<<dim3(Bc * 16 * 16), dim3(256), 0, stream>>>(H, w3b, part);
     rmax_kernel<<<dim3(32), dim3(256), 0, stream>>>(part, b3b, out);
 }
```

Result: slower. 3.068 ms (+22.7%).
